# Optimization experiments

Hardware: AMD Instinct MI355X
Metric: run time of the kernel (lower is better)

## Reference

```python
import jax, jax.numpy as jnp
import numpy as np

B, S, D, H = 2, 2048, 2048, 16
HD = D // H  # head_dim = 128


def rotate_half(x):
    x1, x2 = x[..., : x.shape[-1] // 2], x[..., x.shape[-1] // 2 :]
    return jnp.concatenate((-x2, x1), axis=-1)


def setup_inputs() -> dict:
    key = jax.random.key(0)
    ks = jax.random.split(key, 6)
    x = jax.random.normal(ks[0], (B, S, D), dtype=jnp.float32)
    # RoPE cos/sin tables, shape [B, S, head_dim]
    inv_freq = 1.0 / (10000.0 ** (np.arange(0, HD, 2, dtype=np.float32) / HD))
    t = np.arange(S, dtype=np.float32)
    freqs = np.outer(t, inv_freq)                      # [S, HD/2]
    emb = np.concatenate([freqs, freqs], axis=-1)      # [S, HD]
    cos = jnp.broadcast_to(jnp.cos(emb), (B, S, HD)).astype(jnp.float32)
    sin = jnp.broadcast_to(jnp.sin(emb), (B, S, HD)).astype(jnp.float32)
    attn_mask = jnp.zeros((B, S), dtype=jnp.float32)   # additive 2D mask
    scale = 0.02
    wq = jax.random.normal(ks[1], (D, D), dtype=jnp.float32) * scale
    wk = jax.random.normal(ks[2], (D, D), dtype=jnp.float32) * scale
    wv = jax.random.normal(ks[3], (D, D), dtype=jnp.float32) * scale
    wo = jax.random.normal(ks[4], (D, D), dtype=jnp.float32) * scale
    return {"x": x, "cos": cos, "sin": sin, "attn_mask": attn_mask,
            "wq": wq, "wk": wk, "wv": wv, "wo": wo}


def reference(x, cos, sin, attn_mask, wq, wk, wv, wo):
    b, s, d = x.shape
    # fused-style QKV projections (nn.Linear: y = x @ W.T), reshape to [b,h,s,hd]
    def proj(w):
        return jnp.einsum('bsd,ed->bse', x, w).reshape(b, s, H, HD).transpose(0, 2, 1, 3)
    q, k, v = proj(wq), proj(wk), proj(wv)
    # RoPE: cos/sin [b,s,hd] -> broadcast over heads
    c = cos[:, None, :, :]
    sn = sin[:, None, :, :]
    q = q * c + rotate_half(q) * sn
    k = k * c + rotate_half(k) * sn
    # SDPA with additive 2D mask -> [b,1,1,s]
    scores = jnp.einsum('bhqd,bhkd->bhqk', q, k) / jnp.sqrt(jnp.float32(HD))
    scores = scores + attn_mask[:, None, None, :]
    attn = jax.nn.softmax(scores, axis=-1)
    out = jnp.einsum('bhqk,bhkd->bhqd', attn, v)
    out = out.transpose(0, 2, 1, 3).reshape(b, s, d)
    return jnp.einsum('bsd,ed->bse', out, wo)
```

## Files before the change

kernel.cpp:

```cpp
#include <hip/hip_runtime.h>

#define B_  2
#define S_  2048
#define D_  2048
#define H_  16
#define HD_ 128

typedef float  f32x4  __attribute__((ext_vector_type(4)));
typedef __bf16 bf16x8 __attribute__((ext_vector_type(8)));
typedef __bf16 bf16x4 __attribute__((ext_vector_type(4)));

__device__ __forceinline__ void gl16(const void* g, void* l) {
  __builtin_amdgcn_global_load_lds(
      (const __attribute__((address_space(1))) unsigned int*)g,
      (__attribute__((address_space(3))) unsigned int*)l, 16, 0, 0);
}

__device__ __forceinline__ ushort f2bf(float f) {
  union { float f; unsigned u; } v; v.f = f;
  unsigned r = v.u + 0x7FFFu + ((v.u >> 16) & 1u);
  return (ushort)(r >> 16);
}
__device__ __forceinline__ float bf2f(ushort b) {
  union { unsigned u; float f; } v; v.u = ((unsigned)b) << 16;
  return v.f;
}
__device__ __forceinline__ f32x4 fzero() {
  f32x4 v; v[0] = 0.f; v[1] = 0.f; v[2] = 0.f; v[3] = 0.f; return v;
}
__device__ __forceinline__ float exp2x(float x) {
  return __builtin_amdgcn_exp2f(x);
}

__global__ void cvt4(const float* __restrict__ s, ushort* __restrict__ d, int n4) {
  int i = blockIdx.x * blockDim.x + threadIdx.x;
  if (i >= n4) return;
  float4 v = ((const float4*)s)[i];
  ushort4 o = make_ushort4(f2bf(v.x), f2bf(v.y), f2bf(v.z), f2bf(v.w));
  ((ushort4*)d)[i] = o;
}

template<int MODE>
__global__ __launch_bounds__(256, 2)
void gemm_bt(const ushort* __restrict__ A, const ushort* __restrict__ Bp,
             void* __restrict__ Cp, int M, int N, int K)
{
  __shared__ __align__(16) ushort lds[2][2][128 * 32];
  const int tid  = threadIdx.x;
  const int wave = tid >> 6, lane = tid & 63;
  const int qt = lane >> 4, ln = lane & 15;
  const int wr = wave >> 1, wc = wave & 1;
  const int bm = blockIdx.x * 128, bn = blockIdx.y * 128;

  f32x4 acc[4][4];
#pragma unroll
  for (int a = 0; a < 4; ++a)
#pragma unroll
    for (int b = 0; b < 4; ++b) acc[a][b] = fzero();

  auto stage = [&](int buf, int kt) {
#pragma unroll
    for (int it = 0; it < 2; ++it) {
      int c = it * 256 + tid;
      int row = c >> 2, ch = c & 3;
      int chs = ch ^ ((row >> 1) & 3);
      gl16(A  + (size_t)(bm + row) * K + kt + chs * 8,
           (void*)&lds[buf][0][(it * 256 + wave * 64) * 8]);
      gl16(Bp + (size_t)(bn + row) * K + kt + chs * 8,
           (void*)&lds[buf][1][(it * 256 + wave * 64) * 8]);
    }
  };

  const int nk = K >> 5;
  stage(0, 0);
  int cur = 0;
  for (int kt = 0; kt < nk; ++kt) {
    __syncthreads();
    if (kt + 1 < nk) stage(cur ^ 1, (kt + 1) << 5);
    bf16x8 af[4], bfr[4];
#pragma unroll
    for (int mf = 0; mf < 4; ++mf) {
      int row = wr * 64 + mf * 16 + ln;
      int sl = qt ^ ((row >> 1) & 3);
      af[mf] = *(const bf16x8*)&lds[cur][0][row * 32 + sl * 8];
    }
#pragma unroll
    for (int nf = 0; nf < 4; ++nf) {
      int row = wc * 64 + nf * 16 + ln;
      int sl = qt ^ ((row >> 1) & 3);
      bfr[nf] = *(const bf16x8*)&lds[cur][1][row * 32 + sl * 8];
    }
#pragma unroll
    for (int mf = 0; mf < 4; ++mf)
#pragma unroll
      for (int nf = 0; nf < 4; ++nf)
        acc[mf][nf] = __builtin_amdgcn_mfma_f32_16x16x32_bf16(
            af[mf], bfr[nf], acc[mf][nf], 0, 0, 0);
    cur ^= 1;
  }

#pragma unroll
  for (int mf = 0; mf < 4; ++mf)
#pragma unroll
    for (int nf = 0; nf < 4; ++nf) {
      int m0 = bm + wr * 64 + mf * 16 + qt * 4;
      int n  = bn + wc * 64 + nf * 16 + ln;
#pragma unroll
      for (int i = 0; i < 4; ++i) {
        int m = m0 + i;
        if (MODE == 0) {
          ((float*)Cp)[(size_t)m * N + n] = acc[mf][nf][i];
        } else {
          int b = m >> 11, s = m & 2047;
          int h = n >> 7,  d = n & 127;
          if (MODE == 1)
            ((ushort*)Cp)[(((size_t)b * H_ + h) * S_ + s) * HD_ + d] = f2bf(acc[mf][nf][i]);
          else
            ((ushort*)Cp)[(((size_t)b * H_ + h) * HD_ + d) * S_ + s] = f2bf(acc[mf][nf][i]);
        }
      }
    }
}

__global__ void rope_qk(ushort* __restrict__ Q, ushort* __restrict__ Kt,
                        const float* __restrict__ cs, const float* __restrict__ sn)
{
  int t = blockIdx.x * 256 + threadIdx.x;
  int d  = t & 63;
  int rr = t >> 6;
  int isk = rr >> 16;
  int bhs = rr & 65535;
  int s = bhs & 2047;
  int b = bhs >> 15;
  ushort* P = isk ? Kt : Q;
  size_t ro = (size_t)bhs * HD_;
  float q0 = bf2f(P[ro + d]), q1 = bf2f(P[ro + d + 64]);
  size_t ci = ((size_t)b * S_ + s) * HD_ + d;
  float c0 = cs[ci], s0 = sn[ci], c1 = cs[ci + 64], s1 = sn[ci + 64];
  P[ro + d]      = f2bf(q0 * c0 - q1 * s0);
  P[ro + d + 64] = f2bf(q1 * c1 + q0 * s1);
}

__global__ __launch_bounds__(512, 4)
void flash(const ushort* __restrict__ Q, const ushort* __restrict__ Kk,
           const ushort* __restrict__ VT, const float* __restrict__ mask,
           ushort* __restrict__ O)
{
  __shared__ __align__(16) ushort kt_s[2][64 * 128];
  __shared__ __align__(16) ushort vt_s[2][128 * 64];
  __shared__ __align__(16) ushort pt[8][16 * 64];

  const int tid = threadIdx.x;
  const int wave = tid >> 6, lane = tid & 63;
  const int qt = lane >> 4, ln = lane & 15;
  const int bh = blockIdx.x, b = bh >> 4, h = bh & 15;
  const size_t base  = (size_t)bh * S_ * HD_;
  const size_t baseT = (size_t)bh * HD_ * S_;
  const int q0 = blockIdx.y * 128 + wave * 16;
  const float L2E = 1.4426950408889634f;

  bf16x8 qf[4];
  {
    const ushort* qrow = Q + base + (size_t)(q0 + ln) * HD_;
#pragma unroll
    for (int kk = 0; kk < 4; ++kk)
      qf[kk] = *(const bf16x8*)(qrow + kk * 32 + qt * 8);
  }

  f32x4 accO[8];
#pragma unroll
  for (int i = 0; i < 8; ++i) accO[i] = fzero();
  float mrun = -1e30f;
  float lrun = 0.f;
  const float scale2 = 0.08838834764831845f * L2E;

  auto stageKV = [&](int buf, int k0) {
#pragma unroll
    for (int it = 0; it < 2; ++it) {
      int c = it * 512 + tid;
      int row = c >> 4, ch = c & 15;
      int chs = ch ^ (row & 7);
      gl16(Kk + base + (size_t)(k0 + row) * HD_ + chs * 8,
           (void*)&kt_s[buf][(it * 512 + wave * 64) * 8]);
    }
#pragma unroll
    for (int it = 0; it < 2; ++it) {
      int c = it * 512 + tid;
      int row = c >> 3, ch = c & 7;
      int chs = ch ^ (row & 7);
      gl16(VT + baseT + (size_t)row * S_ + k0 + chs * 8,
           (void*)&vt_s[buf][(it * 512 + wave * 64) * 8]);
    }
  };

  stageKV(0, 0);
  int cur = 0;
  for (int k0 = 0; k0 < S_; k0 += 64) {
    __syncthreads();
    if (k0 + 64 < S_) stageKV(cur ^ 1, k0 + 64);

    f32x4 sc[4];
    __builtin_amdgcn_s_setprio(1);
#pragma unroll
    for (int nf = 0; nf < 4; ++nf) {
      f32x4 a = fzero();
      int row = nf * 16 + ln;
#pragma unroll
      for (int kk = 0; kk < 4; ++kk) {
        int sl = (kk * 4 + qt) ^ (row & 7);
        bf16x8 kf = *(const bf16x8*)&kt_s[cur][row * 128 + sl * 8];
        a = __builtin_amdgcn_mfma_f32_16x16x32_bf16(kf, qf[kk], a, 0, 0, 0);
      }
      sc[nf] = a;
    }
    __builtin_amdgcn_s_setprio(0);

    float sv[4][4];
#pragma unroll
    for (int nf = 0; nf < 4; ++nf) {
      float4 mk = *(const float4*)&mask[(size_t)b * S_ + k0 + nf * 16 + qt * 4];
      sv[nf][0] = sc[nf][0] * scale2 + mk.x * L2E;
      sv[nf][1] = sc[nf][1] * scale2 + mk.y * L2E;
      sv[nf][2] = sc[nf][2] * scale2 + mk.z * L2E;
      sv[nf][3] = sc[nf][3] * scale2 + mk.w * L2E;
    }

    float m = sv[0][0];
#pragma unroll
    for (int nf = 0; nf < 4; ++nf)
#pragma unroll
      for (int i = 0; i < 4; ++i) m = fmaxf(m, sv[nf][i]);
    m = fmaxf(m, __shfl_xor(m, 16));
    m = fmaxf(m, __shfl_xor(m, 32));

    if (__any(m > mrun + 8.f)) {
      float mn = fmaxf(mrun, m);
      float fsc = exp2x(mrun - mn);
      mrun = mn;
      lrun *= fsc;
#pragma unroll
      for (int i = 0; i < 4; ++i) {
        float fq = __shfl(fsc, qt * 4 + i);
#pragma unroll
        for (int nfo = 0; nfo < 8; ++nfo) accO[nfo][i] *= fq;
      }
    }

    float t = 0.f;
#pragma unroll
    for (int nf = 0; nf < 4; ++nf) {
      bf16x4 p4;
#pragma unroll
      for (int i = 0; i < 4; ++i) {
        float p = exp2x(sv[nf][i] - mrun);
        p4[i] = (__bf16)p;
        t += (float)p4[i];
      }
      int g = (nf * 2 + (qt >> 1)) ^ (ln & 7);
      *(bf16x4*)&pt[wave][ln * 64 + g * 8 + (qt & 1) * 4] = p4;
    }
    lrun += t;

    __builtin_amdgcn_s_setprio(1);
#pragma unroll
    for (int kk2 = 0; kk2 < 2; ++kk2) {
      int gr = (kk2 * 4 + qt) ^ (ln & 7);
      bf16x8 pf = *(const bf16x8*)&pt[wave][ln * 64 + gr * 8];
#pragma unroll
      for (int nfo = 0; nfo < 8; ++nfo) {
        int vrow = nfo * 16 + ln;
        int vsl = (kk2 * 4 + qt) ^ (vrow & 7);
        bf16x8 vf = *(const bf16x8*)&vt_s[cur][vrow * 64 + vsl * 8];
        accO[nfo] = __builtin_amdgcn_mfma_f32_16x16x32_bf16(pf, vf, accO[nfo], 0, 0, 0);
      }
    }
    __builtin_amdgcn_s_setprio(0);
    cur ^= 1;
  }

  lrun += __shfl_xor(lrun, 16);
  lrun += __shfl_xor(lrun, 32);
  float inv_own = 1.f / lrun;
  float inv[4];
#pragma unroll
  for (int i = 0; i < 4; ++i) inv[i] = __shfl(inv_own, qt * 4 + i);
#pragma unroll
  for (int nfo = 0; nfo < 8; ++nfo)
#pragma unroll
    for (int i = 0; i < 4; ++i) {
      size_t idx = ((size_t)b * S_ + q0 + qt * 4 + i) * D_ + h * HD_ + nfo * 16 + ln;
      O[idx] = f2bf(accO[nfo][i] * inv[i]);
    }
}

extern "C" void kernel_launch(void* const* d_in, const int* in_sizes, int n_in,
                              void* d_out, int out_size, void* d_ws, size_t ws_size,
                              hipStream_t stream)
{
  if (n_in != 8) return;
  if (in_sizes[0] != 8388608) return;
  if (in_sizes[3] != 4096)    return;
  if (out_size != 8388608) return;
  if (ws_size < (size_t)96 * 1024 * 1024) return;

  const float* x    = (const float*)d_in[0];
  const float* cosb = (const float*)d_in[1];
  const float* sinb = (const float*)d_in[2];
  const float* mask = (const float*)d_in[3];
  const float* wq   = (const float*)d_in[4];
  const float* wk   = (const float*)d_in[5];
  const float* wv   = (const float*)d_in[6];
  const float* wo   = (const float*)d_in[7];

  char* ws = (char*)d_ws;
  ushort* xb  = (ushort*)(ws);
  ushort* wqb = (ushort*)(ws + 16777216);
  ushort* wkb = (ushort*)(ws + 25165824);
  ushort* wvb = (ushort*)(ws + 33554432);
  ushort* wob = (ushort*)(ws + 41943040);
  ushort* Qb  = (ushort*)(ws + 50331648);
  ushort* Kb  = (ushort*)(ws + 67108864);
  ushort* VTb = (ushort*)(ws + 83886080);
  ushort* AOb = xb;

  cvt4<<<8192, 256, 0, stream>>>(x,  xb,  2097152);
  cvt4<<<4096, 256, 0, stream>>>(wq, wqb, 1048576);
  cvt4<<<4096, 256, 0, stream>>>(wk, wkb, 1048576);
  cvt4<<<4096, 256, 0, stream>>>(wv, wvb, 1048576);
  cvt4<<<4096, 256, 0, stream>>>(wo, wob, 1048576);

  dim3 gg(32, 16);
  gemm_bt<1><<<gg, 256, 0, stream>>>(xb, wqb, Qb,  4096, 2048, 2048);
  gemm_bt<1><<<gg, 256, 0, stream>>>(xb, wkb, Kb,  4096, 2048, 2048);
  gemm_bt<3><<<gg, 256, 0, stream>>>(xb, wvb, VTb, 4096, 2048, 2048);

  rope_qk<<<32768, 256, 0, stream>>>(Qb, Kb, cosb, sinb);

  flash<<<dim3(32, 16), 512, 0, stream>>>(Qb, Kb, VTb, mask, AOb);

  gemm_bt<0><<<gg, 256, 0, stream>>>(AOb, wob, d_out, 4096, 2048, 2048);
}
```

Before: 304.3 us.

## Switch flash attention to 32x32x16 MFMA with register-resident P operand

Rewrites the flash attention kernel to use 32x32x16 bf16 MFMA tiles, with 4 waves each handling 32 query rows instead of 8 waves of 16 rows. The softmax probabilities are repacked into the A-operand layout through cross-half lane shuffles rather than a round trip through LDS, so the P scratch buffer goes away. The intent is fewer MFMA issues, fewer LDS reads per FLOP, and less LDS traffic. In exchange each wave holds more accumulator registers and the block has fewer waves to hide latency.

```diff
diff --git a/kernel.cpp b/kernel.cpp
--- a/kernel.cpp
+++ b/kernel.cpp
@@ -7,8 +7,9 @@
 #define HD_ 128
 
 typedef float  f32x4  __attribute__((ext_vector_type(4)));
+typedef float  f32x16 __attribute__((ext_vector_type(16)));
 typedef __bf16 bf16x8 __attribute__((ext_vector_type(8)));
-typedef __bf16 bf16x4 __attribute__((ext_vector_type(4)));
+typedef unsigned int u32;
 
 __device__ __forceinline__ void gl16(const void* g, void* l) {
   __builtin_amdgcn_global_load_lds(
@@ -141,55 +142,56 @@
   P[ro + d + 64] = f2bf(q1 * c1 + q0 * s1);
 }
 
-__global__ __launch_bounds__(512, 4)
+__global__ __launch_bounds__(256, 2)
 void flash(const ushort* __restrict__ Q, const ushort* __restrict__ Kk,
            const ushort* __restrict__ VT, const float* __restrict__ mask,
            ushort* __restrict__ O)
 {
   __shared__ __align__(16) ushort kt_s[2][64 * 128];
   __shared__ __align__(16) ushort vt_s[2][128 * 64];
-  __shared__ __align__(16) ushort pt[8][16 * 64];
 
   const int tid = threadIdx.x;
   const int wave = tid >> 6, lane = tid & 63;
-  const int qt = lane >> 4, ln = lane & 15;
+  const int ln32 = lane & 31, hi = lane >> 5;
   const int bh = blockIdx.x, b = bh >> 4, h = bh & 15;
   const size_t base  = (size_t)bh * S_ * HD_;
   const size_t baseT = (size_t)bh * HD_ * S_;
-  const int q0 = blockIdx.y * 128 + wave * 16;
+  const int q0 = blockIdx.y * 128 + wave * 32;
   const float L2E = 1.4426950408889634f;
-
-  bf16x8 qf[4];
+  const float scale2 = 0.08838834764831845f * L2E;
+
+  bf16x8 qf[8];
   {
-    const ushort* qrow = Q + base + (size_t)(q0 + ln) * HD_;
-#pragma unroll
-    for (int kk = 0; kk < 4; ++kk)
-      qf[kk] = *(const bf16x8*)(qrow + kk * 32 + qt * 8);
+    const ushort* qrow = Q + base + (size_t)(q0 + ln32) * HD_;
+#pragma unroll
+    for (int hd = 0; hd < 8; ++hd)
+      qf[hd] = *(const bf16x8*)(qrow + hd * 16 + hi * 8);
   }
 
-  f32x4 accO[8];
-#pragma unroll
-  for (int i = 0; i < 8; ++i) accO[i] = fzero();
+  f32x16 accO[4];
+#pragma unroll
+  for (int dblk = 0; dblk < 4; ++dblk)
+#pragma unroll
+    for (int i = 0; i < 16; ++i) accO[dblk][i] = 0.f;
   float mrun = -1e30f;
   float lrun = 0.f;
-  const float scale2 = 0.08838834764831845f * L2E;
 
   auto stageKV = [&](int buf, int k0) {
 #pragma unroll
-    for (int it = 0; it < 2; ++it) {
-      int c = it * 512 + tid;
+    for (int it = 0; it < 4; ++it) {
+      int c = it * 256 + tid;
       int row = c >> 4, ch = c & 15;
       int chs = ch ^ (row & 7);
       gl16(Kk + base + (size_t)(k0 + row) * HD_ + chs * 8,
-           (void*)&kt_s[buf][(it * 512 + wave * 64) * 8]);
-    }
-#pragma unroll
-    for (int it = 0; it < 2; ++it) {
-      int c = it * 512 + tid;
+           (void*)&kt_s[buf][(it * 256 + wave * 64) * 8]);
+    }
+#pragma unroll
+    for (int it = 0; it < 4; ++it) {
+      int c = it * 256 + tid;
       int row = c >> 3, ch = c & 7;
       int chs = ch ^ (row & 7);
       gl16(VT + baseT + (size_t)row * S_ + k0 + chs * 8,
-           (void*)&vt_s[buf][(it * 512 + wave * 64) * 8]);
+           (void*)&vt_s[buf][(it * 256 + wave * 64) * 8]);
     }
   };
 
@@ -199,38 +201,41 @@
     __syncthreads();
     if (k0 + 64 < S_) stageKV(cur ^ 1, k0 + 64);
 
-    f32x4 sc[4];
+    f32x16 sc[2];
     __builtin_amdgcn_s_setprio(1);
 #pragma unroll
-    for (int nf = 0; nf < 4; ++nf) {
-      f32x4 a = fzero();
-      int row = nf * 16 + ln;
-#pragma unroll
-      for (int kk = 0; kk < 4; ++kk) {
-        int sl = (kk * 4 + qt) ^ (row & 7);
+    for (int kblk = 0; kblk < 2; ++kblk) {
+      f32x16 a;
+#pragma unroll
+      for (int i = 0; i < 16; ++i) a[i] = 0.f;
+      int row = kblk * 32 + ln32;
+#pragma unroll
+      for (int hd = 0; hd < 8; ++hd) {
+        int sl = (hd * 2 + hi) ^ (row & 7);
         bf16x8 kf = *(const bf16x8*)&kt_s[cur][row * 128 + sl * 8];
-        a = __builtin_amdgcn_mfma_f32_16x16x32_bf16(kf, qf[kk], a, 0, 0, 0);
-      }
-      sc[nf] = a;
+        a = __builtin_amdgcn_mfma_f32_32x32x16_bf16(kf, qf[hd], a, 0, 0, 0);
+      }
+      sc[kblk] = a;
     }
     __builtin_amdgcn_s_setprio(0);
 
-    float sv[4][4];
-#pragma unroll
-    for (int nf = 0; nf < 4; ++nf) {
-      float4 mk = *(const float4*)&mask[(size_t)b * S_ + k0 + nf * 16 + qt * 4];
-      sv[nf][0] = sc[nf][0] * scale2 + mk.x * L2E;
-      sv[nf][1] = sc[nf][1] * scale2 + mk.y * L2E;
-      sv[nf][2] = sc[nf][2] * scale2 + mk.z * L2E;
-      sv[nf][3] = sc[nf][3] * scale2 + mk.w * L2E;
-    }
+    float sv[2][16];
+#pragma unroll
+    for (int kblk = 0; kblk < 2; ++kblk)
+#pragma unroll
+      for (int g = 0; g < 4; ++g) {
+        float4 mk = *(const float4*)&mask[(size_t)b * S_ + k0 + kblk * 32 + g * 8 + hi * 4];
+        sv[kblk][g * 4 + 0] = sc[kblk][g * 4 + 0] * scale2 + mk.x * L2E;
+        sv[kblk][g * 4 + 1] = sc[kblk][g * 4 + 1] * scale2 + mk.y * L2E;
+        sv[kblk][g * 4 + 2] = sc[kblk][g * 4 + 2] * scale2 + mk.z * L2E;
+        sv[kblk][g * 4 + 3] = sc[kblk][g * 4 + 3] * scale2 + mk.w * L2E;
+      }
 
     float m = sv[0][0];
 #pragma unroll
-    for (int nf = 0; nf < 4; ++nf)
-#pragma unroll
-      for (int i = 0; i < 4; ++i) m = fmaxf(m, sv[nf][i]);
-    m = fmaxf(m, __shfl_xor(m, 16));
+    for (int kblk = 0; kblk < 2; ++kblk)
+#pragma unroll
+      for (int i = 0; i < 16; ++i) m = fmaxf(m, sv[kblk][i]);
     m = fmaxf(m, __shfl_xor(m, 32));
 
     if (__any(m > mrun + 8.f)) {
@@ -238,59 +243,88 @@
       float fsc = exp2x(mrun - mn);
       mrun = mn;
       lrun *= fsc;
-#pragma unroll
-      for (int i = 0; i < 4; ++i) {
-        float fq = __shfl(fsc, qt * 4 + i);
-#pragma unroll
-        for (int nfo = 0; nfo < 8; ++nfo) accO[nfo][i] *= fq;
-      }
-    }
-
-    float t = 0.f;
-#pragma unroll
-    for (int nf = 0; nf < 4; ++nf) {
-      bf16x4 p4;
-#pragma unroll
-      for (int i = 0; i < 4; ++i) {
-        float p = exp2x(sv[nf][i] - mrun);
-        p4[i] = (__bf16)p;
-        t += (float)p4[i];
-      }
-      int g = (nf * 2 + (qt >> 1)) ^ (ln & 7);
-      *(bf16x4*)&pt[wave][ln * 64 + g * 8 + (qt & 1) * 4] = p4;
-    }
-    lrun += t;
+      float fq[16];
+#pragma unroll
+      for (int g = 0; g < 4; ++g)
+#pragma unroll
+        for (int j = 0; j < 4; ++j)
+          fq[g * 4 + j] = __shfl(fsc, j + 8 * g + 4 * hi);
+#pragma unroll
+      for (int dblk = 0; dblk < 4; ++dblk)
+#pragma unroll
+        for (int i = 0; i < 16; ++i) accO[dblk][i] *= fq[i];
+    }
+
+    float tsum = 0.f;
+    ushort pb[2][16];
+#pragma unroll
+    for (int kblk = 0; kblk < 2; ++kblk)
+#pragma unroll
+      for (int i = 0; i < 16; ++i) {
+        float p = exp2x(sv[kblk][i] - mrun);
+        __bf16 pq = (__bf16)p;
+        union { __bf16 b; ushort s; } cc; cc.b = pq;
+        pb[kblk][i] = cc.s;
+        tsum += (float)pq;
+      }
+    lrun += tsum;
+
+    bf16x8 pa[4];
+#pragma unroll
+    for (int kblk = 0; kblk < 2; ++kblk) {
+      u32 pk0[4], pk1[4];
+#pragma unroll
+      for (int t = 0; t < 4; ++t) {
+        pk0[t] = (u32)pb[kblk][4 * t]     | ((u32)pb[kblk][4 * t + 1] << 16);
+        pk1[t] = (u32)pb[kblk][4 * t + 2] | ((u32)pb[kblk][4 * t + 3] << 16);
+      }
+#pragma unroll
+      for (int c = 0; c < 2; ++c) {
+        u32 a0 = pk0[2 * c],     a1 = pk1[2 * c];
+        u32 b0 = pk0[2 * c + 1], b1 = pk1[2 * c + 1];
+        u32 s0 = hi ? a0 : b0,   s1 = hi ? a1 : b1;
+        u32 r0 = (u32)__shfl_xor((int)s0, 32);
+        u32 r1 = (u32)__shfl_xor((int)s1, 32);
+        u32 o0 = hi ? b0 : a0,   o1 = hi ? b1 : a1;
+        u32 w[4];
+        w[0] = hi ? r0 : o0;  w[1] = hi ? r1 : o1;
+        w[2] = hi ? o0 : r0;  w[3] = hi ? o1 : r1;
+        pa[kblk * 2 + c] = *(bf16x8*)w;
+      }
+    }
 
     __builtin_amdgcn_s_setprio(1);
 #pragma unroll
-    for (int kk2 = 0; kk2 < 2; ++kk2) {
-      int gr = (kk2 * 4 + qt) ^ (ln & 7);
-      bf16x8 pf = *(const bf16x8*)&pt[wave][ln * 64 + gr * 8];
-#pragma unroll
-      for (int nfo = 0; nfo < 8; ++nfo) {
-        int vrow = nfo * 16 + ln;
-        int vsl = (kk2 * 4 + qt) ^ (vrow & 7);
-        bf16x8 vf = *(const bf16x8*)&vt_s[cur][vrow * 64 + vsl * 8];
-        accO[nfo] = __builtin_amdgcn_mfma_f32_16x16x32_bf16(pf, vf, accO[nfo], 0, 0, 0);
-      }
-    }
+    for (int kk = 0; kk < 4; ++kk)
+#pragma unroll
+      for (int dblk = 0; dblk < 4; ++dblk) {
+        int d = dblk * 32 + ln32;
+        int sl = (kk * 2 + hi) ^ (d & 7);
+        bf16x8 vf = *(const bf16x8*)&vt_s[cur][d * 64 + sl * 8];
+        accO[dblk] = __builtin_amdgcn_mfma_f32_32x32x16_bf16(pa[kk], vf, accO[dblk], 0, 0, 0);
+      }
     __builtin_amdgcn_s_setprio(0);
     cur ^= 1;
   }
 
-  lrun += __shfl_xor(lrun, 16);
   lrun += __shfl_xor(lrun, 32);
   float inv_own = 1.f / lrun;
-  float inv[4];
-#pragma unroll
-  for (int i = 0; i < 4; ++i) inv[i] = __shfl(inv_own, qt * 4 + i);
-#pragma unroll
-  for (int nfo = 0; nfo < 8; ++nfo)
-#pragma unroll
-    for (int i = 0; i < 4; ++i) {
-      size_t idx = ((size_t)b * S_ + q0 + qt * 4 + i) * D_ + h * HD_ + nfo * 16 + ln;
-      O[idx] = f2bf(accO[nfo][i] * inv[i]);
-    }
+  float invv[16];
+#pragma unroll
+  for (int g = 0; g < 4; ++g)
+#pragma unroll
+    for (int j = 0; j < 4; ++j)
+      invv[g * 4 + j] = __shfl(inv_own, j + 8 * g + 4 * hi);
+#pragma unroll
+  for (int dblk = 0; dblk < 4; ++dblk)
+#pragma unroll
+    for (int g = 0; g < 4; ++g)
+#pragma unroll
+      for (int j = 0; j < 4; ++j) {
+        int q = j + 8 * g + 4 * hi;
+        size_t idx = ((size_t)b * S_ + q0 + q) * D_ + h * HD_ + dblk * 32 + ln32;
+        O[idx] = f2bf(accO[dblk][g * 4 + j] * invv[g * 4 + j]);
+      }
 }
 
 extern "C" void kernel_launch(void* const* d_in, const int* in_sizes, int n_in,
@@ -336,7 +370,7 @@
 
   rope_qk<<<32768, 256, 0, stream>>>(Qb, Kb, cosb, sinb);
 
-  flash<<<dim3(32, 16), 512, 0, stream>>>(Qb, Kb, VTb, mask, AOb);
+  flash<<<dim3(32, 16), 256, 0, stream>>>(Qb, Kb, VTb, mask, AOb);
 
   gemm_bt<0><<<gg, 256, 0, stream>>>(AOb, wob, d_out, 4096, 2048, 2048);
 }
```

Result: no change. 305.1 us (+0.2%).
